# Kernel optimization log

Measured on AMD Instinct MI355X. Metric: run time of the kernel, lower is better.

## Reference

```python
import jax, jax.numpy as jnp
import numpy as np

N, D, K = 8192, 256, 64
NEG = -1e9


def setup_inputs() -> dict:
    key = jax.random.key(0)
    ks = jax.random.split(key, 4)
    s = 1.0 / np.sqrt(D)
    return {
        "example_features": jax.random.normal(ks[0], (N, D), dtype=jnp.float32),
        "Wq": jax.random.normal(ks[1], (D, D), dtype=jnp.float32) * s,
        "bq": jnp.zeros((D,), dtype=jnp.float32),
        "Wk": jax.random.normal(ks[2], (D, D), dtype=jnp.float32) * s,
        "bk": jnp.zeros((D,), dtype=jnp.float32),
        "Wv": jax.random.normal(ks[3], (D, D), dtype=jnp.float32) * s,
        "bv": jnp.zeros((D,), dtype=jnp.float32),
        "temperature": jnp.ones((1,), dtype=jnp.float32),
        "k": K,
    }


def reference(example_features, Wq, bq, Wk, bk, Wv, bv, temperature, k):
    n, d = example_features.shape
    # QKV projections (torch Linear: x @ W.T + b)
    Q = example_features @ Wq.T + bq
    Km = example_features @ Wk.T + bk
    V = example_features @ Wv.T + bv
    # dense scores with learned temperature
    scores = (Q @ Km.T) / (temperature[0] * jnp.sqrt(jnp.float32(d)))
    # self-exclusion mask on the diagonal
    idx = jnp.arange(n)
    scores = scores.at[idx, idx].set(NEG)
    # per-row top-k thresholding (k < N-1 in this config)
    topk_vals = jax.lax.top_k(scores, k)[0]          # (N, k)
    threshold = topk_vals[:, -1:]                     # kth largest per row
    scores = jnp.where(scores < threshold, NEG, scores)
    attn = jax.nn.softmax(scores, axis=1)
    return attn @ V
```

## Files before the change

kernel.cpp:

```cpp
#include <hip/hip_runtime.h>
#include <math.h>

#define NN 8192
#define DD 256
#define TOPK 64
#define CAP 96
#define CCAP 256
#define CRMAX 2048
#define NEGVAL (-1000000000.0f)

typedef _Float16 f16;
typedef f16  f16x4 __attribute__((ext_vector_type(4)));
typedef f16  f16x8 __attribute__((ext_vector_type(8)));
typedef float f32x4 __attribute__((ext_vector_type(4)));

__global__ __launch_bounds__(256)
void gemm_qkv(const float* __restrict__ X,
              const float* __restrict__ Wq, const float* __restrict__ bq,
              const float* __restrict__ Wk, const float* __restrict__ bk,
              const float* __restrict__ Wv, const float* __restrict__ bv,
              f16* __restrict__ Qs, f16* __restrict__ Ks,
              float* __restrict__ Vf)
{
  __shared__ float As[32][68];
  __shared__ float Bs[3][32][68];
  const int t  = threadIdx.x;
  const int tm = t & 15;
  const int tn = t >> 4;
  const int m0 = blockIdx.x * 64;
  const int n0 = blockIdx.y * 64;

  float acc[3][4][4];
#pragma unroll
  for (int g = 0; g < 3; ++g)
#pragma unroll
    for (int i = 0; i < 4; ++i)
#pragma unroll
      for (int j = 0; j < 4; ++j) acc[g][i][j] = 0.0f;

  for (int k0 = 0; k0 < DD; k0 += 32) {
    __syncthreads();
#pragma unroll
    for (int i = 0; i < 2; ++i) {
      const int slot = t + i * 256;
      const int row  = slot >> 3;
      const int c4   = (slot & 7) << 2;
      float4 av = *(const float4*)(X + (size_t)(m0 + row) * DD + k0 + c4);
      As[c4 + 0][row] = av.x; As[c4 + 1][row] = av.y;
      As[c4 + 2][row] = av.z; As[c4 + 3][row] = av.w;
      float4 q4 = *(const float4*)(Wq + (size_t)(n0 + row) * DD + k0 + c4);
      Bs[0][c4 + 0][row] = q4.x; Bs[0][c4 + 1][row] = q4.y;
      Bs[0][c4 + 2][row] = q4.z; Bs[0][c4 + 3][row] = q4.w;
      float4 k4 = *(const float4*)(Wk + (size_t)(n0 + row) * DD + k0 + c4);
      Bs[1][c4 + 0][row] = k4.x; Bs[1][c4 + 1][row] = k4.y;
      Bs[1][c4 + 2][row] = k4.z; Bs[1][c4 + 3][row] = k4.w;
      float4 v4 = *(const float4*)(Wv + (size_t)(n0 + row) * DD + k0 + c4);
      Bs[2][c4 + 0][row] = v4.x; Bs[2][c4 + 1][row] = v4.y;
      Bs[2][c4 + 2][row] = v4.z; Bs[2][c4 + 3][row] = v4.w;
    }
    __syncthreads();
#pragma unroll
    for (int kk = 0; kk < 32; ++kk) {
      float a[4];
      *(float4*)&a[0] = *(const float4*)&As[kk][tm * 4];
      float b0[4], b1[4], b2[4];
      *(float4*)&b0[0] = *(const float4*)&Bs[0][kk][tn * 4];
      *(float4*)&b1[0] = *(const float4*)&Bs[1][kk][tn * 4];
      *(float4*)&b2[0] = *(const float4*)&Bs[2][kk][tn * 4];
#pragma unroll
      for (int i = 0; i < 4; ++i)
#pragma unroll
        for (int j = 0; j < 4; ++j) {
          acc[0][i][j] = fmaf(a[i], b0[j], acc[0][i][j]);
          acc[1][i][j] = fmaf(a[i], b1[j], acc[1][i][j]);
          acc[2][i][j] = fmaf(a[i], b2[j], acc[2][i][j]);
        }
    }
  }

#pragma unroll
  for (int r = 0; r < 4; ++r) {
    const int grow  = m0 + tm * 4 + r;
    const int gcol0 = n0 + tn * 4;
    {
      f16x4 h4, l4;
#pragma unroll
      for (int c = 0; c < 4; ++c) {
        const float val = acc[0][r][c] + bq[gcol0 + c];
        f16 h = (f16)val;
        h4[c] = h;
        l4[c] = (f16)(val - (float)h);
      }
      f16* base = Qs + (size_t)grow * 768 + gcol0;
      *(f16x4*)(base)       = h4;
      *(f16x4*)(base + 256) = h4;
      *(f16x4*)(base + 512) = l4;
    }
    {
      f16x4 h4, l4;
#pragma unroll
      for (int c = 0; c < 4; ++c) {
        const float val = acc[1][r][c] + bk[gcol0 + c];
        f16 h = (f16)val;
        h4[c] = h;
        l4[c] = (f16)(val - (float)h);
      }
      f16* base = Ks + (size_t)grow * 768 + gcol0;
      *(f16x4*)(base)       = h4;
      *(f16x4*)(base + 256) = l4;
      *(f16x4*)(base + 512) = h4;
    }
    {
      float val[4];
#pragma unroll
      for (int c = 0; c < 4; ++c)
        val[c] = acc[2][r][c] + bv[gcol0 + c];
      *(float4*)(Vf + (size_t)grow * DD + gcol0) =
          make_float4(val[0], val[1], val[2], val[3]);
    }
  }
}

typedef __attribute__((address_space(1))) const void GV;
typedef __attribute__((address_space(3))) void LV;
__device__ __forceinline__ void gl_lds16(const void* g, void* l) {
  __builtin_amdgcn_global_load_lds((GV*)g, (LV*)l, 16, 0, 0);
}

__global__ __launch_bounds__(256)
void gemm_scores_f16(const f16* __restrict__ Aq, const f16* __restrict__ Bk,
                     float* __restrict__ C, const float* __restrict__ temp,
                     int rowOff)
{
  __shared__ __align__(16) f16 As[128 * 64];
  __shared__ __align__(16) f16 Bs[128 * 64];
  const int t  = threadIdx.x;
  const int l  = t & 63;
  const int w  = t >> 6;
  const int wr = w >> 1;
  const int wc = w & 1;
  const int m0 = blockIdx.x * 128;
  const int n0 = blockIdx.y * 128;

  f32x4 acc[4][4];
#pragma unroll
  for (int m = 0; m < 4; ++m)
#pragma unroll
    for (int n = 0; n < 4; ++n) acc[m][n] = (f32x4){0.f, 0.f, 0.f, 0.f};

  const int lr = l >> 3;
  const int lk = (l & 7) * 8;
  const int fr = l & 15;
  const int fg = l >> 4;

  for (int k0 = 0; k0 < 768; k0 += 64) {
    __syncthreads();
#pragma unroll
    for (int i = 0; i < 4; ++i) {
      const int seg = w * 4 + i;
      gl_lds16(Aq + (size_t)(m0 + seg * 8 + lr) * 768 + k0 + lk, &As[seg * 512]);
      gl_lds16(Bk + (size_t)(n0 + seg * 8 + lr) * 768 + k0 + lk, &Bs[seg * 512]);
    }
    __syncthreads();
#pragma unroll
    for (int kk = 0; kk < 2; ++kk) {
      f16x8 af[4], bf[4];
#pragma unroll
      for (int m = 0; m < 4; ++m)
        af[m] = *(const f16x8*)&As[(wr * 64 + m * 16 + fr) * 64 + kk * 32 + fg * 8];
#pragma unroll
      for (int n = 0; n < 4; ++n)
        bf[n] = *(const f16x8*)&Bs[(wc * 64 + n * 16 + fr) * 64 + kk * 32 + fg * 8];
#pragma unroll
      for (int m = 0; m < 4; ++m)
#pragma unroll
        for (int n = 0; n < 4; ++n)
          acc[m][n] = __builtin_amdgcn_mfma_f32_16x16x32_f16(af[m], bf[n], acc[m][n], 0, 0, 0);
    }
  }

  const float invts = 1.0f / (temp[0] * 16.0f);
#pragma unroll
  for (int m = 0; m < 4; ++m)
#pragma unroll
    for (int n = 0; n < 4; ++n) {
      const int gcol = n0 + wc * 64 + n * 16 + fr;
#pragma unroll
      for (int j = 0; j < 4; ++j) {
        const int lrow = m0 + wr * 64 + m * 16 + fg * 4 + j;
        float x = acc[m][n][j] * invts;
        if (rowOff + lrow == gcol) x = NEGVAL;
        C[(size_t)lrow * NN + gcol] = x;
      }
    }
}

__global__ __launch_bounds__(256)
void topk_softmax3(const float* __restrict__ Sc, int rowOff,
                   float* __restrict__ wts, int* __restrict__ idx,
                   int* __restrict__ cnt)
{
  __shared__ unsigned hist[256];
  __shared__ float    candv[CCAP];
  __shared__ float    pb[CAP];
  __shared__ int      jb[CAP];
  __shared__ float    wmax[4], wsum[4];
  __shared__ int      wtot[4];
  __shared__ int      sB;
  __shared__ unsigned uT;

  const int t = threadIdx.x;
  const int l = t & 63;
  const int w = t >> 6;
  const int grow = rowOff + blockIdx.x;
  const float* srow = Sc + (size_t)blockIdx.x * NN;

  float v[32];
#pragma unroll
  for (int c = 0; c < 8; ++c) {
    float4 f = *(const float4*)(srow + ((size_t)c * 256 + t) * 4);
    v[c * 4 + 0] = f.x; v[c * 4 + 1] = f.y; v[c * 4 + 2] = f.z; v[c * 4 + 3] = f.w;
  }

  float lm = -3.0e38f;
#pragma unroll
  for (int r = 0; r < 32; ++r) lm = fmaxf(lm, v[r]);
#pragma unroll
  for (int off = 32; off; off >>= 1) lm = fmaxf(lm, __shfl_xor(lm, off));
  if (l == 0) wmax[w] = lm;
  __syncthreads();
  const float m = fmaxf(fmaxf(wmax[0], wmax[1]), fmaxf(wmax[2], wmax[3]));

  float lo = m - 2.5f;
  float invw = 0.0f;
  int B = -1;
  for (int iter = 0; iter < 8; ++iter) {
    hist[t] = 0u;
    __syncthreads();
    invw = 256.0f / (m - lo);
#pragma unroll
    for (int r = 0; r < 32; ++r) {
      float s = v[r];
      if (s >= lo) {
        int b = (int)((s - lo) * invw);
        b = (b > 255) ? 255 : b;
        atomicAdd(&hist[b], 1u);
      }
    }
    __syncthreads();
    const int c = (int)hist[t];
    int x = c;
#pragma unroll
    for (int off = 1; off < 64; off <<= 1) {
      int y = __shfl_down(x, off);
      if (l + off < 64) x += y;
    }
    if (l == 0) wtot[w] = x;
    __syncthreads();
    int hi = 0;
#pragma unroll
    for (int ww = 0; ww < 4; ++ww) if (ww > w) hi += wtot[ww];
    const int S = x + hi;
    const int total = wtot[0] + wtot[1] + wtot[2] + wtot[3];
    if (total >= TOPK) {
      if (S >= TOPK && S - c < TOPK) sB = t;
      __syncthreads();
      B = sB;
      break;
    }
    __syncthreads();
    lo = m - 2.5f * (float)(2 << iter);
  }
  if (B < 0) B = 0;

  int cc = 0;
#pragma unroll
  for (int r = 0; r < 32; ++r) {
    float s = v[r];
    if (s >= lo) {
      int b = (int)((s - lo) * invw);
      b = (b > 255) ? 255 : b;
      if (b >= B) ++cc;
    }
  }
  {
    int x = cc;
#pragma unroll
    for (int off = 1; off < 64; off <<= 1) {
      int y = __shfl_up(x, off);
      if (l >= off) x += y;
    }
    if (l == 63) wtot[w] = x;
    __syncthreads();
    int lowsum = 0;
#pragma unroll
    for (int ww = 0; ww < 4; ++ww) if (ww < w) lowsum += wtot[ww];
    int base = lowsum + x - cc;
    const int ctotal = wtot[0] + wtot[1] + wtot[2] + wtot[3];
#pragma unroll
    for (int r = 0; r < 32; ++r) {
      float s = v[r];
      if (s >= lo) {
        int b = (int)((s - lo) * invw);
        b = (b > 255) ? 255 : b;
        if (b >= B) {
          if (base < CCAP) candv[base] = s;
          ++base;
        }
      }
    }
    __syncthreads();
    const int L = (ctotal < CCAP) ? ctotal : CCAP;

    if (t == 0) uT = 0xFFFFFFFFu;
    __syncthreads();
    for (int i = t; i < L; i += 256) {
      float vi = candv[i];
      int g = 0;
      for (int j = 0; j < L; ++j) g += (candv[j] > vi) ? 1 : 0;
      if (g <= TOPK - 1) {
        unsigned ub = __float_as_uint(vi);
        unsigned u = (ub & 0x80000000u) ? ~ub : (ub | 0x80000000u);
        atomicMin(&uT, u);
      }
    }
    __syncthreads();
  }
  const unsigned uth = uT;
  const float T = __uint_as_float((uth & 0x80000000u) ? (uth & 0x7FFFFFFFu) : ~uth);

  int myc = 0;
#pragma unroll
  for (int r = 0; r < 32; ++r) myc += (v[r] >= T) ? 1 : 0;
  int x2 = myc;
#pragma unroll
  for (int off = 1; off < 64; off <<= 1) {
    int y = __shfl_up(x2, off);
    if (l >= off) x2 += y;
  }
  if (l == 63) wtot[w] = x2;
  __syncthreads();
  int lowsum2 = 0;
#pragma unroll
  for (int ww = 0; ww < 4; ++ww) if (ww < w) lowsum2 += wtot[ww];
  int base = lowsum2 + x2 - myc;
  const int total2 = wtot[0] + wtot[1] + wtot[2] + wtot[3];
#pragma unroll
  for (int r = 0; r < 32; ++r) {
    if (v[r] >= T) {
      if (base < CAP) {
        pb[base] = __expf(v[r] - m);
        jb[base] = ((r >> 2) * 256 + t) * 4 + (r & 3);
      }
      ++base;
    }
  }
  __syncthreads();
  const int L2 = (total2 < CAP) ? total2 : CAP;

  float ps = 0.0f;
  for (int i = t; i < L2; i += 256) ps += pb[i];
#pragma unroll
  for (int off = 32; off; off >>= 1) ps += __shfl_xor(ps, off);
  if (l == 0) wsum[w] = ps;
  __syncthreads();
  const float inv = 1.0f / (wsum[0] + wsum[1] + wsum[2] + wsum[3]);
  for (int i = t; i < L2; i += 256) {
    wts[(size_t)grow * CAP + i] = pb[i] * inv;
    idx[(size_t)grow * CAP + i] = jb[i];
  }
  if (t == 0) cnt[grow] = L2;
}

__global__ __launch_bounds__(256)
void sparse_av(const float* __restrict__ V, const float* __restrict__ wts,
               const int* __restrict__ idx, const int* __restrict__ cnt,
               float* __restrict__ out)
{
  __shared__ float wl[CAP];
  __shared__ int   jl[CAP];
  const int t = threadIdx.x;
  const int row = blockIdx.x;
  const int L = cnt[row];
  if (t < CAP && t < L) {
    wl[t] = wts[(size_t)row * CAP + t];
    jl[t] = idx[(size_t)row * CAP + t];
  }
  __syncthreads();
  float acc = 0.0f;
  for (int i = 0; i < L; ++i)
    acc = fmaf(wl[i], V[(size_t)jl[i] * DD + t], acc);
  out[(size_t)row * DD + t] = acc;
}

extern "C" void kernel_launch(void* const* d_in, const int* in_sizes, int n_in,
                              void* d_out, int out_size, void* d_ws, size_t ws_size,
                              hipStream_t stream)
{
  const float* X    = (const float*)d_in[0];
  const float* Wq   = (const float*)d_in[1];
  const float* bq   = (const float*)d_in[2];
  const float* Wk   = (const float*)d_in[3];
  const float* bk   = (const float*)d_in[4];
  const float* Wv   = (const float*)d_in[5];
  const float* bv   = (const float*)d_in[6];
  const float* temp = (const float*)d_in[7];
  float* out = (float*)d_out;
  float* ws  = (float*)d_ws;

  const size_t avail = ws_size / sizeof(float);

  const size_t szV   = (size_t)NN * DD;
  const size_t szHL  = (size_t)NN * 768 / 2;
  const size_t szWts = (size_t)NN * CAP;
  const size_t szIdx = (size_t)NN * CAP;
  const size_t szCnt = NN;
  const size_t fixed = szV + 2 * szHL + szWts + szIdx + szCnt;

  size_t o = 0;
  float* Vbuf = ws + o; o += szV;
  f16*   Qs   = (f16*)(ws + o); o += szHL;
  f16*   Ks   = (f16*)(ws + o); o += szHL;
  float* wts  = ws + o; o += szWts;
  int*   idxb = (int*)(ws + o); o += szIdx;
  int*   cntb = (int*)(ws + o); o += szCnt;

  if (avail <= fixed + (size_t)128 * NN) return;
  int CR = (int)(((avail - fixed) / NN) / 128) * 128;
  if (CR > CRMAX) CR = CRMAX;
  if (CR > NN) CR = NN;
  float* Sc = ws + o;

  dim3 blk(256);

  gemm_qkv<<<dim3(NN/64, 4), blk, 0, stream>>>(X, Wq, bq, Wk, bk, Wv, bv,
                                               Qs, Ks, Vbuf);

  for (int r0 = 0; r0 < NN; r0 += CR) {
    const int rows = (NN - r0 < CR) ? (NN - r0) : CR;
    gemm_scores_f16<<<dim3(rows/128, NN/128), blk, 0, stream>>>(
        Qs + (size_t)r0 * 768, Ks, Sc, temp, r0);
    topk_softmax3<<<dim3(rows), blk, 0, stream>>>(Sc, r0, wts, idxb, cntb);
  }

  sparse_av<<<dim3(NN), blk, 0, stream>>>(Vbuf, wts, idxb, cntb, out);
}
```

Before: 378.7 us.

## Enlarge score GEMM tile to 256x256 with double-buffered swizzled LDS

Rewrites the scores GEMM to use 512-thread blocks computing 256x256 output tiles. It double-buffers the LDS staging with async global-to-LDS loads overlapped with MFMA compute, XOR-swizzles the k offsets to avoid LDS bank conflicts, and raises wave priority around the MFMA bursts. Row chunking on the host is changed to multiples of 256 to match. The larger per-wave accumulator (8x4 fragments) raises register pressure and limits occupancy to one block per CU, and fewer blocks are launched per chunk.

```diff
diff --git a/kernel.cpp b/kernel.cpp
--- a/kernel.cpp
+++ b/kernel.cpp
@@ -127,67 +127,96 @@
   __builtin_amdgcn_global_load_lds((GV*)g, (LV*)l, 16, 0, 0);
 }
 
-__global__ __launch_bounds__(256)
+__global__ __launch_bounds__(512, 1)
 void gemm_scores_f16(const f16* __restrict__ Aq, const f16* __restrict__ Bk,
                      float* __restrict__ C, const float* __restrict__ temp,
                      int rowOff)
 {
-  __shared__ __align__(16) f16 As[128 * 64];
-  __shared__ __align__(16) f16 Bs[128 * 64];
+  __shared__ __align__(16) f16 lds[2][2][256 * 64];
+
   const int t  = threadIdx.x;
   const int l  = t & 63;
   const int w  = t >> 6;
-  const int wr = w >> 1;
-  const int wc = w & 1;
-  const int m0 = blockIdx.x * 128;
-  const int n0 = blockIdx.y * 128;
-
-  f32x4 acc[4][4];
-#pragma unroll
-  for (int m = 0; m < 4; ++m)
-#pragma unroll
-    for (int n = 0; n < 4; ++n) acc[m][n] = (f32x4){0.f, 0.f, 0.f, 0.f};
-
-  const int lr = l >> 3;
-  const int lk = (l & 7) * 8;
+  const int wm = w >> 2;
+  const int wn = w & 3;
+  const int m0 = blockIdx.x * 256;
+  const int n0 = blockIdx.y * 256;
   const int fr = l & 15;
   const int fg = l >> 4;
 
-  for (int k0 = 0; k0 < 768; k0 += 64) {
-    __syncthreads();
-#pragma unroll
-    for (int i = 0; i < 4; ++i) {
-      const int seg = w * 4 + i;
-      gl_lds16(Aq + (size_t)(m0 + seg * 8 + lr) * 768 + k0 + lk, &As[seg * 512]);
-      gl_lds16(Bk + (size_t)(n0 + seg * 8 + lr) * 768 + k0 + lk, &Bs[seg * 512]);
-    }
-    __syncthreads();
+  const int srow = w * 8 + (l >> 3);
+  const int koff = ((l & 7) ^ (l >> 3)) * 8;
+
+  f32x4 acc[8][4];
+#pragma unroll
+  for (int m = 0; m < 8; ++m)
+#pragma unroll
+    for (int n = 0; n < 4; ++n) acc[m][n] = (f32x4){0.f, 0.f, 0.f, 0.f};
+
+  auto stage = [&](int d, int kt) {
+    const int kb = kt * 64 + koff;
+#pragma unroll
+    for (int j = 0; j < 4; ++j)
+      gl_lds16(Aq + (size_t)(m0 + j * 64 + srow) * 768 + kb,
+               &lds[d][0][j * 4096 + w * 512]);
+#pragma unroll
+    for (int j = 0; j < 4; ++j)
+      gl_lds16(Bk + (size_t)(n0 + j * 64 + srow) * 768 + kb,
+               &lds[d][1][j * 4096 + w * 512]);
+  };
+
+  stage(0, 0);
+
+#pragma unroll 1
+  for (int kt = 0; kt < 12; ++kt) {
+    const int d = kt & 1;
+    if (kt + 1 < 12) {
+      stage(d ^ 1, kt + 1);
+      asm volatile("s_waitcnt vmcnt(8)" ::: "memory");
+    } else {
+      asm volatile("s_waitcnt vmcnt(0)" ::: "memory");
+    }
+    __builtin_amdgcn_s_barrier();
+    __builtin_amdgcn_sched_barrier(0);
+
+    const f16* Ab = &lds[d][0][0];
+    const f16* Bb = &lds[d][1][0];
 #pragma unroll
     for (int kk = 0; kk < 2; ++kk) {
-      f16x8 af[4], bf[4];
-#pragma unroll
-      for (int m = 0; m < 4; ++m)
-        af[m] = *(const f16x8*)&As[(wr * 64 + m * 16 + fr) * 64 + kk * 32 + fg * 8];
+      const int g = ((kk * 4 + fg) ^ (fr & 7)) * 8;
+      f16x8 bf[4];
 #pragma unroll
       for (int n = 0; n < 4; ++n)
-        bf[n] = *(const f16x8*)&Bs[(wc * 64 + n * 16 + fr) * 64 + kk * 32 + fg * 8];
-#pragma unroll
-      for (int m = 0; m < 4; ++m)
-#pragma unroll
-        for (int n = 0; n < 4; ++n)
-          acc[m][n] = __builtin_amdgcn_mfma_f32_16x16x32_f16(af[m], bf[n], acc[m][n], 0, 0, 0);
-    }
+        bf[n] = *(const f16x8*)&Bb[(wn * 64 + n * 16 + fr) * 64 + g];
+#pragma unroll
+      for (int mh = 0; mh < 2; ++mh) {
+        f16x8 af[4];
+#pragma unroll
+        for (int i = 0; i < 4; ++i)
+          af[i] = *(const f16x8*)&Ab[(wm * 128 + (mh * 4 + i) * 16 + fr) * 64 + g];
+        __builtin_amdgcn_s_setprio(1);
+#pragma unroll
+        for (int i = 0; i < 4; ++i)
+#pragma unroll
+          for (int n = 0; n < 4; ++n)
+            acc[mh * 4 + i][n] = __builtin_amdgcn_mfma_f32_16x16x32_f16(
+                af[i], bf[n], acc[mh * 4 + i][n], 0, 0, 0);
+        __builtin_amdgcn_s_setprio(0);
+      }
+    }
+    __builtin_amdgcn_sched_barrier(0);
+    __builtin_amdgcn_s_barrier();
   }
 
   const float invts = 1.0f / (temp[0] * 16.0f);
 #pragma unroll
-  for (int m = 0; m < 4; ++m)
+  for (int m = 0; m < 8; ++m)
 #pragma unroll
     for (int n = 0; n < 4; ++n) {
-      const int gcol = n0 + wc * 64 + n * 16 + fr;
+      const int gcol = n0 + wn * 64 + n * 16 + fr;
 #pragma unroll
       for (int j = 0; j < 4; ++j) {
-        const int lrow = m0 + wr * 64 + m * 16 + fg * 4 + j;
+        const int lrow = m0 + wm * 128 + m * 16 + fg * 4 + j;
         float x = acc[m][n][j] * invts;
         if (rowOff + lrow == gcol) x = NEGVAL;
         C[(size_t)lrow * NN + gcol] = x;
@@ -425,20 +454,21 @@
   int*   idxb = (int*)(ws + o); o += szIdx;
   int*   cntb = (int*)(ws + o); o += szCnt;
 
-  if (avail <= fixed + (size_t)128 * NN) return;
-  int CR = (int)(((avail - fixed) / NN) / 128) * 128;
+  if (avail <= fixed + (size_t)256 * NN) return;
+  int CR = (int)(((avail - fixed) / NN) / 256) * 256;
   if (CR > CRMAX) CR = CRMAX;
   if (CR > NN) CR = NN;
   float* Sc = ws + o;
 
   dim3 blk(256);
+  dim3 blk2(512);
 
   gemm_qkv<<<dim3(NN/64, 4), blk, 0, stream>>>(X, Wq, bq, Wk, bk, Wv, bv,
                                                Qs, Ks, Vbuf);
 
   for (int r0 = 0; r0 < NN; r0 += CR) {
     const int rows = (NN - r0 < CR) ? (NN - r0) : CR;
-    gemm_scores_f16<<<dim3(rows/128, NN/128), blk, 0, stream>>>(
+    gemm_scores_f16<<<dim3(rows/256, NN/256), blk2, 0, stream>>>(
         Qs + (size_t)r0 * 768, Ks, Sc, temp, r0);
     topk_softmax3<<<dim3(rows), blk, 0, stream>>>(Sc, r0, wts, idxb, cntb);
   }
```

New measurement: 332.3 us. 12.3% less time.
